# Performance work log

Measured on AMD Instinct MI355X. Metric: run time of the kernel, lower is better.

The kernel has to match this reference:

```python
import jax, jax.numpy as jnp
import numpy as np

TAU = 0.95
MARGIN = 1.0
NUM_NEG = 1

B, S = 4096, 4096
N_RERANK = 8192


def setup_inputs() -> dict:
    key = jax.random.key(0)
    k1, k2, k3 = jax.random.split(key, 3)
    rerank_y = jax.random.normal(k1, (N_RERANK, 1), dtype=jnp.float32)
    # probabilities in (0,1]; keep away from 0 since the loss takes log
    cut_y = jax.random.uniform(k2, (B, S, 1), dtype=jnp.float32, minval=1e-4, maxval=1.0)
    rerank_label = jnp.ones((B, 1), dtype=jnp.float32)  # unused (overwritten by ones in source)
    cut_label = jax.random.randint(k3, (B, S), 0, 2, dtype=jnp.int32)
    return {"rerank_y": rerank_y, "cut_y": cut_y, "rerank_label": rerank_label, "cut_label": cut_label}


def _f1_weights(cut_label):
    # Vectorized Metric_for_Loss.f1(labels[i], j): F1 at cut depth j+1.
    lab = cut_label.astype(jnp.float32)                      # [B,S]
    cum = jnp.cumsum(lab, axis=1)                            # relevant docs within top j+1
    k = jnp.arange(1, lab.shape[1] + 1, dtype=jnp.float32)   # cut depth
    total = jnp.sum(lab, axis=1, keepdims=True)              # total relevant per list
    prec = cum / k
    rec = jnp.where(total > 0, cum / jnp.maximum(total, 1.0), 0.0)
    den = prec + rec
    return jnp.where(den > 0, 2.0 * prec * rec / den, 0.0)   # [B,S]


def _attncut_loss(cut_y, cut_label):
    out2d = jnp.squeeze(cut_y, axis=2)                       # [B,S]
    r = _f1_weights(cut_label)
    # Faithful to source: q = exp(r/tau) is summed into norm_factor, then q := 1/norm_factor
    norm = jnp.sum(jnp.exp(r / TAU), axis=1, keepdims=True)  # [B,1]
    q = 1.0 / norm
    loss_mat = jnp.log(out2d) * q
    return -jnp.sum(loss_mat) / out2d.shape[0]


def _rerank_loss(rerank_y):
    y_pos = rerank_y[:: NUM_NEG + 1, :]                      # [B,1]
    y_neg = rerank_y[1 :: NUM_NEG + 1, :]                    # [B,1] (num_neg=1 -> cat of one)
    y_neg = jnp.mean(y_neg, axis=-1, keepdims=True)
    # margin_ranking_loss with y=1, reduction='mean'
    return jnp.mean(jnp.maximum(0.0, -(y_pos - y_neg) + MARGIN))


def reference(rerank_y, cut_y, rerank_label, cut_label):
    return _attncut_loss(cut_y, cut_label) + _rerank_loss(rerank_y)
```

## Files before the change

### kernel.cpp

```cpp
#include <hip/hip_runtime.h>

#define NROWS 4096
#define NCOLS 4096
#define TAU 0.95f
#define MARGIN 1.0f
#define LN2F 0.6931471805599453f

__global__ __launch_bounds__(256) void fused_kernel(
    const float* __restrict__ cut_y, const int* __restrict__ cut_label,
    float* __restrict__ norm_out, float* __restrict__ logsum_out) {
  const int wid = threadIdx.x >> 6;
  const int lane = threadIdx.x & 63;
  const int row = (blockIdx.x >> 1) * 4 + wid;

  if ((blockIdx.x & 1) == 0) {
    const float4* Yp = (const float4*)(cut_y + (size_t)row * NCOLS);
    float s0 = 0.f, s1 = 0.f, s2 = 0.f, s3 = 0.f;
#define LOG4(V) (__log2f((V).x) + __log2f((V).y) + __log2f((V).z) + __log2f((V).w))
#pragma unroll
    for (int i = 0; i < 4; ++i) {
      const float4 a = Yp[lane + 64 * (4 * i + 0)];
      const float4 b = Yp[lane + 64 * (4 * i + 1)];
      const float4 c = Yp[lane + 64 * (4 * i + 2)];
      const float4 d = Yp[lane + 64 * (4 * i + 3)];
      s0 += LOG4(a);
      s1 += LOG4(b);
      s2 += LOG4(c);
      s3 += LOG4(d);
    }
#undef LOG4
    float s = (s0 + s1) + (s2 + s3);
#pragma unroll
    for (int off = 32; off > 0; off >>= 1) s += __shfl_down(s, off, 64);
    if (lane == 0) logsum_out[row] = s * LN2F;
  } else {
    const int4* Lp = (const int4*)(cut_label + (size_t)row * NCOLS) + lane * 16;
    unsigned mlo = 0u, mhi = 0u;
#pragma unroll
    for (int i = 0; i < 4; ++i) {
      const int4 a = Lp[4 * i + 0];
      const int4 b = Lp[4 * i + 1];
      const int4 c = Lp[4 * i + 2];
      const int4 d = Lp[4 * i + 3];
      const unsigned na = (unsigned)a.x | ((unsigned)a.y << 1) |
                          ((unsigned)a.z << 2) | ((unsigned)a.w << 3);
      const unsigned nb = (unsigned)b.x | ((unsigned)b.y << 1) |
                          ((unsigned)b.z << 2) | ((unsigned)b.w << 3);
      const unsigned nc = (unsigned)c.x | ((unsigned)c.y << 1) |
                          ((unsigned)c.z << 2) | ((unsigned)c.w << 3);
      const unsigned nd = (unsigned)d.x | ((unsigned)d.y << 1) |
                          ((unsigned)d.z << 2) | ((unsigned)d.w << 3);
      const unsigned group = na | (nb << 4) | (nc << 8) | (nd << 12);
      if (i < 2)
        mlo |= group << (16 * i);
      else
        mhi |= group << (16 * (i - 2));
    }
    const int cnt = __popc(mlo) + __popc(mhi);

    int x = cnt;
#pragma unroll
    for (int off = 1; off < 64; off <<= 1) {
      const int v = __shfl_up(x, off, 64);
      if (lane >= off) x += v;
    }
    const int Ttot = __shfl(x, 63, 64);
    int c = x - cnt;

    const float Tf = (float)Ttot;
    const float C2 = 2.0f / (TAU * LN2F);
    const float kb = (float)(lane * 64 + 1) + Tf;
    float acc0 = 0.f, acc1 = 0.f;
#pragma unroll
    for (int j = 0; j < 64; ++j) {
      const unsigned w = (j < 32) ? mlo : mhi;
      c += (int)((w >> (j & 31)) & 1u);
      const float term =
          __builtin_amdgcn_exp2f(__fdividef((float)c * C2, kb + (float)j));
      if (j & 1)
        acc1 += term;
      else
        acc0 += term;
    }
    float norm = acc0 + acc1;
#pragma unroll
    for (int off = 32; off > 0; off >>= 1) norm += __shfl_down(norm, off, 64);
    if (lane == 0) norm_out[row] = norm;
  }
}

__global__ __launch_bounds__(256) void finish_kernel(
    const float* __restrict__ norms, const float* __restrict__ logsums,
    const float* __restrict__ rerank_y, float* __restrict__ out) {
  const int t = threadIdx.x;
  const int lane = t & 63, wid = t >> 6;

  float acc = 0.f;
  const float4* n4 = (const float4*)norms;
  const float4* l4 = (const float4*)logsums;
#pragma unroll
  for (int i = 0; i < 4; ++i) {
    const float4 n = n4[t + 256 * i];
    const float4 l = l4[t + 256 * i];
    acc += __fdividef(l.x, n.x) + __fdividef(l.y, n.y) +
           __fdividef(l.z, n.z) + __fdividef(l.w, n.w);
  }
  acc *= -(1.0f / (float)NROWS);

  float racc = 0.f;
  const float4* y4 = (const float4*)rerank_y;
#pragma unroll
  for (int i = 0; i < 8; ++i) {
    const float4 v = y4[t + 256 * i];
    racc += fmaxf(0.f, MARGIN - (v.x - v.y));
    racc += fmaxf(0.f, MARGIN - (v.z - v.w));
  }
  acc += racc * (1.0f / 4096.0f);

#pragma unroll
  for (int off = 32; off > 0; off >>= 1) acc += __shfl_down(acc, off, 64);
  __shared__ float ws[4];
  if (lane == 0) ws[wid] = acc;
  __syncthreads();
  if (t == 0) out[0] = (ws[0] + ws[1]) + (ws[2] + ws[3]);
}

extern "C" void kernel_launch(void* const* d_in, const int* in_sizes, int n_in,
                              void* d_out, int out_size, void* d_ws, size_t ws_size,
                              hipStream_t stream) {
  const float* rerank_y = (const float*)d_in[0];
  const float* cut_y = (const float*)d_in[1];
  const int* cut_label = (const int*)d_in[3];
  float* out = (float*)d_out;
  float* norms = (float*)d_ws;
  float* logsums = (float*)d_ws + NROWS;

  fused_kernel<<<2 * (NROWS / 4), 256, 0, stream>>>(cut_y, cut_label, norms,
                                                    logsums);
  finish_kernel<<<1, 256, 0, stream>>>(norms, logsums, rerank_y, out);
}
```

Baseline: 163.2 us.

## Process two rows per wave with prefetch and interleaved coalesced label layout

Each wave now handles two rows: the loads for the second row are issued while the first row's log or norm work is still running, which is meant to hide memory latency. Label loads switch from a per-lane contiguous chunk to a lane-strided, coalesced pattern. This needs a segmented prefix scan over eight packed 16-bit counters instead of one. Block indexing is changed to group the log and label roles in runs of eight blocks, and the grid is halved. The cost is more registers, which may lower occupancy, and a more complex scan.

```diff
diff --git a/kernel.cpp b/kernel.cpp
--- a/kernel.cpp
+++ b/kernel.cpp
@@ -6,86 +6,143 @@
 #define MARGIN 1.0f
 #define LN2F 0.6931471805599453f
 
+__device__ __forceinline__ void norm_row(unsigned mlo, unsigned mhi,
+                                         const unsigned* __restrict__ p,
+                                         int lane, float* __restrict__ dst) {
+  unsigned h[8];
+#pragma unroll
+  for (int i = 0; i < 8; ++i) h[i] = p[i];
+#pragma unroll
+  for (int off = 1; off < 64; off <<= 1) {
+    unsigned v[8];
+#pragma unroll
+    for (int i = 0; i < 8; ++i) v[i] = __shfl_up(h[i], off, 64);
+    if (lane >= off) {
+#pragma unroll
+      for (int i = 0; i < 8; ++i) h[i] += v[i];
+    }
+  }
+  unsigned ex[8], tot[8];
+#pragma unroll
+  for (int i = 0; i < 8; ++i) ex[i] = h[i] - p[i];
+#pragma unroll
+  for (int i = 0; i < 8; ++i) tot[i] = __shfl(h[i], 63, 64);
+
+  const unsigned tsum = ((tot[0] + tot[1]) + (tot[2] + tot[3])) +
+                        ((tot[4] + tot[5]) + (tot[6] + tot[7]));
+  const float Tf = (float)((tsum & 0xFFFFu) + (tsum >> 16));
+
+  const float C2 = 2.0f / (TAU * LN2F);
+  float acc0 = 0.f, acc1 = 0.f;
+  unsigned run = 0;
+#pragma unroll
+  for (int s = 0; s < 16; ++s) {
+    const unsigned nib = ((s < 8) ? (mlo >> (4 * s)) : (mhi >> (4 * (s - 8)))) & 0xFu;
+    const unsigned exl = (ex[s >> 1] >> (16 * (s & 1))) & 0xFFFFu;
+    int c = (int)(run + exl);
+    const float kb = (float)(s * 256 + lane * 4 + 1) + Tf;
+    c += (int)(nib & 1u);
+    acc0 += __builtin_amdgcn_exp2f(__fdividef((float)c * C2, kb));
+    c += (int)((nib >> 1) & 1u);
+    acc1 += __builtin_amdgcn_exp2f(__fdividef((float)c * C2, kb + 1.0f));
+    c += (int)((nib >> 2) & 1u);
+    acc0 += __builtin_amdgcn_exp2f(__fdividef((float)c * C2, kb + 2.0f));
+    c += (int)((nib >> 3) & 1u);
+    acc1 += __builtin_amdgcn_exp2f(__fdividef((float)c * C2, kb + 3.0f));
+    run += (tot[s >> 1] >> (16 * (s & 1))) & 0xFFFFu;
+  }
+  float norm = acc0 + acc1;
+#pragma unroll
+  for (int off = 32; off > 0; off >>= 1) norm += __shfl_down(norm, off, 64);
+  if (lane == 0) *dst = norm;
+}
+
+__device__ __forceinline__ void pack_row(const int4* __restrict__ buf,
+                                         unsigned& mlo, unsigned& mhi,
+                                         unsigned* __restrict__ p) {
+  unsigned nib[16];
+#pragma unroll
+  for (int s = 0; s < 16; ++s)
+    nib[s] = (unsigned)buf[s].x | ((unsigned)buf[s].y << 1) |
+             ((unsigned)buf[s].z << 2) | ((unsigned)buf[s].w << 3);
+  mlo = 0u;
+  mhi = 0u;
+#pragma unroll
+  for (int s = 0; s < 8; ++s) mlo |= nib[s] << (4 * s);
+#pragma unroll
+  for (int s = 8; s < 16; ++s) mhi |= nib[s] << (4 * (s - 8));
+#pragma unroll
+  for (int i = 0; i < 8; ++i)
+    p[i] = (unsigned)__popc(nib[2 * i]) | ((unsigned)__popc(nib[2 * i + 1]) << 16);
+}
+
 __global__ __launch_bounds__(256) void fused_kernel(
     const float* __restrict__ cut_y, const int* __restrict__ cut_label,
     float* __restrict__ norm_out, float* __restrict__ logsum_out) {
+  const int g = blockIdx.x;
+  const int role = (g >> 3) & 1;
+  const int idx = (g & 7) | ((g >> 4) << 3);
   const int wid = threadIdx.x >> 6;
   const int lane = threadIdx.x & 63;
-  const int row = (blockIdx.x >> 1) * 4 + wid;
+  const int r0 = (idx * 4 + wid) * 2;
 
-  if ((blockIdx.x & 1) == 0) {
-    const float4* Yp = (const float4*)(cut_y + (size_t)row * NCOLS);
-    float s0 = 0.f, s1 = 0.f, s2 = 0.f, s3 = 0.f;
-#define LOG4(V) (__log2f((V).x) + __log2f((V).y) + __log2f((V).z) + __log2f((V).w))
+  if (role == 0) {
+    const float4* Y0 = (const float4*)(cut_y + (size_t)r0 * NCOLS) + lane;
+    const float4* Y1 = (const float4*)(cut_y + (size_t)(r0 + 1) * NCOLS) + lane;
+    float4 a[8], b[8];
 #pragma unroll
-    for (int i = 0; i < 4; ++i) {
-      const float4 a = Yp[lane + 64 * (4 * i + 0)];
-      const float4 b = Yp[lane + 64 * (4 * i + 1)];
-      const float4 c = Yp[lane + 64 * (4 * i + 2)];
-      const float4 d = Yp[lane + 64 * (4 * i + 3)];
-      s0 += LOG4(a);
-      s1 += LOG4(b);
-      s2 += LOG4(c);
-      s3 += LOG4(d);
+    for (int s = 0; s < 8; ++s) a[s] = Y0[s * 64];
+#pragma unroll
+    for (int s = 0; s < 8; ++s) b[s] = Y0[(s + 8) * 64];
+    float t0 = 0.f, t1 = 0.f, t2 = 0.f, t3 = 0.f;
+#pragma unroll
+    for (int s = 0; s < 8; ++s) {
+      t0 += __log2f(a[s].x); t1 += __log2f(a[s].y);
+      t2 += __log2f(a[s].z); t3 += __log2f(a[s].w);
     }
-#undef LOG4
-    float s = (s0 + s1) + (s2 + s3);
 #pragma unroll
-    for (int off = 32; off > 0; off >>= 1) s += __shfl_down(s, off, 64);
-    if (lane == 0) logsum_out[row] = s * LN2F;
+    for (int s = 0; s < 8; ++s) a[s] = Y1[s * 64];
+#pragma unroll
+    for (int s = 0; s < 8; ++s) {
+      t0 += __log2f(b[s].x); t1 += __log2f(b[s].y);
+      t2 += __log2f(b[s].z); t3 += __log2f(b[s].w);
+    }
+#pragma unroll
+    for (int s = 0; s < 8; ++s) b[s] = Y1[(s + 8) * 64];
+    float srow = (t0 + t1) + (t2 + t3);
+#pragma unroll
+    for (int off = 32; off > 0; off >>= 1) srow += __shfl_down(srow, off, 64);
+    if (lane == 0) logsum_out[r0] = srow * LN2F;
+    t0 = t1 = t2 = t3 = 0.f;
+#pragma unroll
+    for (int s = 0; s < 8; ++s) {
+      t0 += __log2f(a[s].x); t1 += __log2f(a[s].y);
+      t2 += __log2f(a[s].z); t3 += __log2f(a[s].w);
+    }
+#pragma unroll
+    for (int s = 0; s < 8; ++s) {
+      t0 += __log2f(b[s].x); t1 += __log2f(b[s].y);
+      t2 += __log2f(b[s].z); t3 += __log2f(b[s].w);
+    }
+    srow = (t0 + t1) + (t2 + t3);
+#pragma unroll
+    for (int off = 32; off > 0; off >>= 1) srow += __shfl_down(srow, off, 64);
+    if (lane == 0) logsum_out[r0 + 1] = srow * LN2F;
   } else {
-    const int4* Lp = (const int4*)(cut_label + (size_t)row * NCOLS) + lane * 16;
-    unsigned mlo = 0u, mhi = 0u;
+    const int4* L0 = (const int4*)(cut_label + (size_t)r0 * NCOLS) + lane;
+    const int4* L1 = (const int4*)(cut_label + (size_t)(r0 + 1) * NCOLS) + lane;
+    int4 buf[16];
 #pragma unroll
-    for (int i = 0; i < 4; ++i) {
-      const int4 a = Lp[4 * i + 0];
-      const int4 b = Lp[4 * i + 1];
-      const int4 c = Lp[4 * i + 2];
-      const int4 d = Lp[4 * i + 3];
-      const unsigned na = (unsigned)a.x | ((unsigned)a.y << 1) |
-                          ((unsigned)a.z << 2) | ((unsigned)a.w << 3);
-      const unsigned nb = (unsigned)b.x | ((unsigned)b.y << 1) |
-                          ((unsigned)b.z << 2) | ((unsigned)b.w << 3);
-      const unsigned nc = (unsigned)c.x | ((unsigned)c.y << 1) |
-                          ((unsigned)c.z << 2) | ((unsigned)c.w << 3);
-      const unsigned nd = (unsigned)d.x | ((unsigned)d.y << 1) |
-                          ((unsigned)d.z << 2) | ((unsigned)d.w << 3);
-      const unsigned group = na | (nb << 4) | (nc << 8) | (nd << 12);
-      if (i < 2)
-        mlo |= group << (16 * i);
-      else
-        mhi |= group << (16 * (i - 2));
-    }
-    const int cnt = __popc(mlo) + __popc(mhi);
+    for (int s = 0; s < 16; ++s) buf[s] = L0[s * 64];
 
-    int x = cnt;
+    unsigned mlo, mhi, p[8];
+    pack_row(buf, mlo, mhi, p);
 #pragma unroll
-    for (int off = 1; off < 64; off <<= 1) {
-      const int v = __shfl_up(x, off, 64);
-      if (lane >= off) x += v;
-    }
-    const int Ttot = __shfl(x, 63, 64);
-    int c = x - cnt;
+    for (int s = 0; s < 16; ++s) buf[s] = L1[s * 64];
+    norm_row(mlo, mhi, p, lane, norm_out + r0);
 
-    const float Tf = (float)Ttot;
-    const float C2 = 2.0f / (TAU * LN2F);
-    const float kb = (float)(lane * 64 + 1) + Tf;
-    float acc0 = 0.f, acc1 = 0.f;
-#pragma unroll
-    for (int j = 0; j < 64; ++j) {
-      const unsigned w = (j < 32) ? mlo : mhi;
-      c += (int)((w >> (j & 31)) & 1u);
-      const float term =
-          __builtin_amdgcn_exp2f(__fdividef((float)c * C2, kb + (float)j));
-      if (j & 1)
-        acc1 += term;
-      else
-        acc0 += term;
-    }
-    float norm = acc0 + acc1;
-#pragma unroll
-    for (int off = 32; off > 0; off >>= 1) norm += __shfl_down(norm, off, 64);
-    if (lane == 0) norm_out[row] = norm;
+    pack_row(buf, mlo, mhi, p);
+    norm_row(mlo, mhi, p, lane, norm_out + r0 + 1);
   }
 }
 
@@ -135,7 +192,6 @@
   float* norms = (float*)d_ws;
   float* logsums = (float*)d_ws + NROWS;
 
-  fused_kernel<<<2 * (NROWS / 4), 256, 0, stream>>>(cut_y, cut_label, norms,
-                                                    logsums);
+  fused_kernel<<<1024, 256, 0, stream>>>(cut_y, cut_label, norms, logsums);
   finish_kernel<<<1, 256, 0, stream>>>(norms, logsums, rerank_y, out);
 }
```

New measurement: 157.3 us. -3.6%, faster.
